# Kernel tuning notes

Measured on AMD Instinct MI355X. Metric: run time of the kernel, lower is better.

Reference implementation:

```python
import jax, jax.numpy as jnp
import numpy as np

INPUT_DIM = 128
DEPTH = 6
HIDDEN = 64
NUM_INNER = 2 ** DEPTH - 1  # 63
NUM_LEAVES = 2 ** DEPTH     # 64


def setup_inputs() -> dict:
    key = jax.random.key(0)
    ks = jax.random.split(key, 6)
    x = jax.random.normal(ks[0], (65536, INPUT_DIM), dtype=jnp.float32)
    s1 = 1.0 / np.sqrt(INPUT_DIM)
    s2 = 1.0 / np.sqrt(HIDDEN)
    W1 = jax.random.uniform(ks[1], (NUM_INNER, INPUT_DIM, HIDDEN), minval=-s1, maxval=s1, dtype=jnp.float32)
    b1 = jax.random.uniform(ks[2], (NUM_INNER, HIDDEN), minval=-s1, maxval=s1, dtype=jnp.float32)
    W2 = jax.random.uniform(ks[3], (NUM_INNER, HIDDEN), minval=-s2, maxval=s2, dtype=jnp.float32)
    b2 = jax.random.uniform(ks[4], (NUM_INNER,), minval=-s2, maxval=s2, dtype=jnp.float32)
    leaf = jax.random.normal(ks[5], (NUM_LEAVES, 1), dtype=jnp.float32)
    return {"x": x, "W1": W1, "b1": b1, "W2": W2, "b2": b2, "leaf": leaf}


def reference(x, W1, b1, W2, b2, leaf):
    # All inner-node MLPs as one batched GEMM pair: [B, N] node probabilities
    h = jax.nn.relu(jnp.einsum('bi,nih->bnh', x, W1) + b1)      # [B, N, H]
    probs = jax.nn.sigmoid(jnp.einsum('bnh,nh->bn', h, W2) + b2)  # [B, N]

    # Original code walks node_idx = 2*node_idx+1 unconditionally, so the chain
    # of used node indices is 2^k - 1 for k = 0..depth-1.
    chain = jnp.array([2 ** k - 1 for k in range(DEPTH)], dtype=jnp.int32)
    p_chain = probs[:, chain]  # [B, D]

    # Bit k (LSB first) of leaf index selects p (bit=1) vs 1-p (bit=0)
    leaves = np.arange(NUM_LEAVES)
    bits = jnp.asarray(((leaves[:, None] >> np.arange(DEPTH)[None, :]) & 1).astype(np.float32))  # [L, D]

    # path_probs[b, l] = prod_k ( bits[l,k]*p + (1-bits[l,k])*(1-p) )
    factors = bits[None, :, :] * p_chain[:, None, :] + (1.0 - bits[None, :, :]) * (1.0 - p_chain[:, None, :])  # [B, L, D]
    path_probs = jnp.prod(factors, axis=-1)  # [B, L]

    return (path_probs @ leaf)[:, 0]  # [B]
```

## Files before the change

kernel.cpp:

```cpp
#include <hip/hip_runtime.h>

typedef __attribute__((ext_vector_type(4))) float f32x4;
typedef __attribute__((ext_vector_type(8))) short bf16x8;
typedef __attribute__((ext_vector_type(4))) unsigned int u32x4;

#define IDIM    128
#define HID     64
#define TDEPTH  6
#define WROWS   32
#define NWAVES  8
#define BLOCK   (NWAVES * 64)
#define MROWS   (WROWS * NWAVES)
#define NODE_ELEMS 8192
#define WFRAG_ELEMS (TDEPTH * NODE_ELEMS)

__device__ __forceinline__ unsigned short f2bf(float f) {
    unsigned int u = __builtin_bit_cast(unsigned int, f);
    unsigned int r = (u + 0x7FFFu + ((u >> 16) & 1u)) >> 16;
    return (unsigned short)r;
}

__device__ __forceinline__ unsigned int f2bf_pk(float f0, float f1) {
    unsigned int u0 = __builtin_bit_cast(unsigned int, f0);
    unsigned int u1 = __builtin_bit_cast(unsigned int, f1);
    unsigned int t0 = u0 + 0x7FFFu + ((u0 >> 16) & 1u);
    unsigned int t1 = u1 + 0x7FFFu + ((u1 >> 16) & 1u);
    return (t1 & 0xFFFF0000u) | (t0 >> 16);
}

__global__ void prep_wfrag(const float* __restrict__ W1, unsigned short* __restrict__ wfrag) {
    int idx = blockIdx.x * 256 + threadIdx.x;
    if (idx >= WFRAG_ELEMS) return;
    int j    = idx & 7;
    int lane = (idx >> 3) & 63;
    int ks   = (idx >> 9) & 3;
    int ht   = (idx >> 11) & 3;
    int nd   = idx >> 13;
    int node = (1 << nd) - 1;
    int k    = ks * 32 + (lane >> 4) * 8 + j;
    int hid  = ht * 16 + (lane & 15);
    wfrag[idx] = f2bf(W1[((size_t)node * IDIM + k) * HID + hid]);
}

template <bool USE_WS>
__global__ __launch_bounds__(BLOCK, 2)
void sdt_kernel(const float* __restrict__ x, const float* __restrict__ W1,
                const float* __restrict__ b1, const float* __restrict__ W2,
                const float* __restrict__ b2, const float* __restrict__ leaf,
                const unsigned short* __restrict__ wfrag, float* __restrict__ out) {
    __shared__ __align__(16) unsigned short bs[TDEPTH * NODE_ELEMS];
    __shared__ float b1s[TDEPTH][HID];
    __shared__ float w2s[TDEPTH][HID];
    __shared__ float b2s[8];
    __shared__ float leaf_lds[64];

    const int tid  = threadIdx.x;
    const int wave = tid >> 6;
    const int lane = tid & 63;
    const int lcol = lane & 15;
    const int lq   = lane >> 4;
    const int m0   = blockIdx.x * MROWS + wave * WROWS;

    const float* xb = x + (size_t)(m0 + lcol) * IDIM + lq * 8;
    float4 araw[2][4][2];
    #pragma unroll
    for (int bg = 0; bg < 2; bg++)
        #pragma unroll
        for (int ks = 0; ks < 4; ks++) {
            const float4* ap = reinterpret_cast<const float4*>(
                xb + (size_t)(bg * 16) * IDIM + ks * 32);
            araw[bg][ks][0] = ap[0];
            araw[bg][ks][1] = ap[1];
        }

    if (USE_WS) {
        const u32x4* src = reinterpret_cast<const u32x4*>(wfrag);
        u32x4* dst = reinterpret_cast<u32x4*>(&bs[0]);
        #pragma unroll
        for (int i = 0; i < (WFRAG_ELEMS * 2 / 16) / BLOCK; i++)
            dst[tid + i * BLOCK] = src[tid + i * BLOCK];
    } else {
        for (int e = tid; e < WFRAG_ELEMS; e += BLOCK) {
            int j = e & 7, ln = (e >> 3) & 63, ks = (e >> 9) & 3,
                ht = (e >> 11) & 3, nd = e >> 13;
            int node = (1 << nd) - 1;
            int k    = ks * 32 + (ln >> 4) * 8 + j;
            int hid  = ht * 16 + (ln & 15);
            bs[e] = f2bf(W1[((size_t)node * IDIM + k) * HID + hid]);
        }
    }
    for (int i = tid; i < TDEPTH * HID; i += BLOCK) {
        int nd = i >> 6, col = i & 63, node = (1 << nd) - 1;
        b1s[nd][col] = b1[node * HID + col];
        w2s[nd][col] = W2[node * HID + col];
    }
    if (tid < 6)  b2s[tid] = b2[(1 << tid) - 1];
    if (tid < 64) leaf_lds[tid] = leaf[tid];

    bf16x8 xfrag[2][4];
    #pragma unroll
    for (int bg = 0; bg < 2; bg++)
        #pragma unroll
        for (int ks = 0; ks < 4; ks++) {
            float4 v0 = araw[bg][ks][0], v1 = araw[bg][ks][1];
            u32x4 pk;
            pk[0] = f2bf_pk(v0.x, v0.y);
            pk[1] = f2bf_pk(v0.z, v0.w);
            pk[2] = f2bf_pk(v1.x, v1.y);
            pk[3] = f2bf_pk(v1.z, v1.w);
            xfrag[bg][ks] = __builtin_bit_cast(bf16x8, pk);
        }

    __syncthreads();

    float pq[2][TDEPTH];

    #pragma unroll
    for (int nd = 0; nd < TDEPTH; nd++) {
        f32x4 acc[2][4];
        #pragma unroll
        for (int bg = 0; bg < 2; bg++)
            #pragma unroll
            for (int ht = 0; ht < 4; ht++)
                acc[bg][ht] = (f32x4){0.f, 0.f, 0.f, 0.f};
        #pragma unroll
        for (int ks = 0; ks < 4; ks++) {
            bf16x8 awf[4];
            #pragma unroll
            for (int ht = 0; ht < 4; ht++)
                awf[ht] = *reinterpret_cast<const bf16x8*>(
                    &bs[(nd * 16 + ht * 4 + ks) * 512 + lane * 8]);
            #pragma unroll
            for (int bg = 0; bg < 2; bg++)
                #pragma unroll
                for (int ht = 0; ht < 4; ht++)
                    acc[bg][ht] = __builtin_amdgcn_mfma_f32_16x16x32_bf16(
                        awf[ht], xfrag[bg][ks], acc[bg][ht], 0, 0, 0);
        }

        f32x4 b1q[4], w2q[4];
        #pragma unroll
        for (int ht = 0; ht < 4; ht++) {
            b1q[ht] = *reinterpret_cast<const f32x4*>(&b1s[nd][ht * 16 + lq * 4]);
            w2q[ht] = *reinterpret_cast<const f32x4*>(&w2s[nd][ht * 16 + lq * 4]);
        }
        const float bias2 = b2s[nd];
        #pragma unroll
        for (int bg = 0; bg < 2; bg++) {
            float s = 0.f;
            #pragma unroll
            for (int ht = 0; ht < 4; ht++)
                #pragma unroll
                for (int r = 0; r < 4; r++) {
                    float v = acc[bg][ht][r] + b1q[ht][r];
                    v = v > 0.f ? v : 0.f;
                    s += v * w2q[ht][r];
                }
            s += __shfl_xor(s, 16, 64);
            s += __shfl_xor(s, 32, 64);
            pq[bg][nd] = 1.f / (1.f + __expf(-(s + bias2)));
        }
    }

    #pragma unroll
    for (int bg = 0; bg < 2; bg++) {
        float q0 = pq[bg][0], q1 = pq[bg][1], q2 = pq[bg][2];
        float q3 = pq[bg][3], p4 = pq[bg][4], p5 = pq[bg][5];
        float acc_out = 0.f;
        #pragma unroll
        for (int ch = 0; ch < 4; ch++) {
            float f4 = (ch & 1) ? p4 : 1.f - p4;
            float f5 = (ch & 2) ? p5 : 1.f - p5;
            const float* lf = leaf_lds + ch * 16;
            float tt[8];
            #pragma unroll
            for (int j = 0; j < 8; j++) {
                float a = lf[2 * j], b = lf[2 * j + 1];
                tt[j] = a + q0 * (b - a);
            }
            #pragma unroll
            for (int j = 0; j < 4; j++) tt[j] = tt[2 * j] + q1 * (tt[2 * j + 1] - tt[2 * j]);
            #pragma unroll
            for (int j = 0; j < 2; j++) tt[j] = tt[2 * j] + q2 * (tt[2 * j + 1] - tt[2 * j]);
            float s = tt[0] + q3 * (tt[1] - tt[0]);
            acc_out += f4 * f5 * s;
        }
        if (lq == 0)
            out[(size_t)m0 + bg * 16 + lcol] = acc_out;
    }
}

extern "C" void kernel_launch(void* const* d_in, const int* in_sizes, int n_in,
                              void* d_out, int out_size, void* d_ws, size_t ws_size,
                              hipStream_t stream) {
    const float* x    = (const float*)d_in[0];
    const float* W1   = (const float*)d_in[1];
    const float* b1   = (const float*)d_in[2];
    const float* W2   = (const float*)d_in[3];
    const float* b2   = (const float*)d_in[4];
    const float* leaf = (const float*)d_in[5];
    float* out = (float*)d_out;

    const int Bn = in_sizes[0] / IDIM;
    const int nblocks = Bn / MROWS;

    if (ws_size >= (size_t)WFRAG_ELEMS * sizeof(unsigned short)) {
        unsigned short* wfrag = (unsigned short*)d_ws;
        prep_wfrag<<<(WFRAG_ELEMS + 255) / 256, 256, 0, stream>>>(W1, wfrag);
        sdt_kernel<true><<<nblocks, BLOCK, 0, stream>>>(x, W1, b1, W2, b2, leaf, wfrag, out);
    } else {
        sdt_kernel<false><<<nblocks, BLOCK, 0, stream>>>(x, W1, b1, W2, b2, leaf, nullptr, out);
    }
}
```

Before: 94.04 us.

## Halve LDS weight buffer with two-phase node staging and smaller blocks

Shrinks the shared-memory weight buffer to hold three tree levels at a time. The second half of the weights is prefetched into registers and written to LDS after the first three nodes are computed. Blocks drop from 8 to 4 waves, and launch bounds now target 3 blocks per CU, to raise occupancy with the smaller LDS footprint. In exchange it adds two extra barriers, register pressure from the prefetched half, and more blocks that each reload the weights.

```diff
diff --git a/kernel.cpp b/kernel.cpp
--- a/kernel.cpp
+++ b/kernel.cpp
@@ -8,11 +8,13 @@
 #define HID     64
 #define TDEPTH  6
 #define WROWS   32
-#define NWAVES  8
+#define NWAVES  4
 #define BLOCK   (NWAVES * 64)
 #define MROWS   (WROWS * NWAVES)
 #define NODE_ELEMS 8192
+#define HALF_ELEMS (3 * NODE_ELEMS)
 #define WFRAG_ELEMS (TDEPTH * NODE_ELEMS)
+#define HALF_VEC (HALF_ELEMS * 2 / 16 / BLOCK)
 
 __device__ __forceinline__ unsigned short f2bf(float f) {
     unsigned int u = __builtin_bit_cast(unsigned int, f);
@@ -43,12 +45,12 @@
 }
 
 template <bool USE_WS>
-__global__ __launch_bounds__(BLOCK, 2)
+__global__ __launch_bounds__(BLOCK, 3)
 void sdt_kernel(const float* __restrict__ x, const float* __restrict__ W1,
                 const float* __restrict__ b1, const float* __restrict__ W2,
                 const float* __restrict__ b2, const float* __restrict__ leaf,
                 const unsigned short* __restrict__ wfrag, float* __restrict__ out) {
-    __shared__ __align__(16) unsigned short bs[TDEPTH * NODE_ELEMS];
+    __shared__ __align__(16) unsigned short bs[HALF_ELEMS];
     __shared__ float b1s[TDEPTH][HID];
     __shared__ float w2s[TDEPTH][HID];
     __shared__ float b2s[8];
@@ -73,14 +75,20 @@
             araw[bg][ks][1] = ap[1];
         }
 
+    u32x4 sB[HALF_VEC];
     if (USE_WS) {
-        const u32x4* src = reinterpret_cast<const u32x4*>(wfrag);
+        const u32x4* srcB = reinterpret_cast<const u32x4*>(wfrag + HALF_ELEMS);
+        #pragma unroll
+        for (int i = 0; i < HALF_VEC; i++) sB[i] = srcB[tid + i * BLOCK];
+    }
+
+    if (USE_WS) {
+        const u32x4* srcA = reinterpret_cast<const u32x4*>(wfrag);
         u32x4* dst = reinterpret_cast<u32x4*>(&bs[0]);
         #pragma unroll
-        for (int i = 0; i < (WFRAG_ELEMS * 2 / 16) / BLOCK; i++)
-            dst[tid + i * BLOCK] = src[tid + i * BLOCK];
+        for (int i = 0; i < HALF_VEC; i++) dst[tid + i * BLOCK] = srcA[tid + i * BLOCK];
     } else {
-        for (int e = tid; e < WFRAG_ELEMS; e += BLOCK) {
+        for (int e = tid; e < HALF_ELEMS; e += BLOCK) {
             int j = e & 7, ln = (e >> 3) & 63, ks = (e >> 9) & 3,
                 ht = (e >> 11) & 3, nd = e >> 13;
             int node = (1 << nd) - 1;
@@ -89,6 +97,7 @@
             bs[e] = f2bf(W1[((size_t)node * IDIM + k) * HID + hid]);
         }
     }
+
     for (int i = tid; i < TDEPTH * HID; i += BLOCK) {
         int nd = i >> 6, col = i & 63, node = (1 << nd) - 1;
         b1s[nd][col] = b1[node * HID + col];
@@ -115,8 +124,7 @@
 
     float pq[2][TDEPTH];
 
-    #pragma unroll
-    for (int nd = 0; nd < TDEPTH; nd++) {
+    auto compute = [&](int nd, int ndl) {
         f32x4 acc[2][4];
         #pragma unroll
         for (int bg = 0; bg < 2; bg++)
@@ -129,7 +137,7 @@
             #pragma unroll
             for (int ht = 0; ht < 4; ht++)
                 awf[ht] = *reinterpret_cast<const bf16x8*>(
-                    &bs[(nd * 16 + ht * 4 + ks) * 512 + lane * 8]);
+                    &bs[(ndl * 16 + ht * 4 + ks) * 512 + lane * 8]);
             #pragma unroll
             for (int bg = 0; bg < 2; bg++)
                 #pragma unroll
@@ -137,7 +145,6 @@
                     acc[bg][ht] = __builtin_amdgcn_mfma_f32_16x16x32_bf16(
                         awf[ht], xfrag[bg][ks], acc[bg][ht], 0, 0, 0);
         }
-
         f32x4 b1q[4], w2q[4];
         #pragma unroll
         for (int ht = 0; ht < 4; ht++) {
@@ -160,7 +167,28 @@
             s += __shfl_xor(s, 32, 64);
             pq[bg][nd] = 1.f / (1.f + __expf(-(s + bias2)));
         }
-    }
+    };
+
+    compute(0, 0); compute(1, 1); compute(2, 2);
+    __syncthreads();
+
+    if (USE_WS) {
+        u32x4* dst = reinterpret_cast<u32x4*>(&bs[0]);
+        #pragma unroll
+        for (int i = 0; i < HALF_VEC; i++) dst[tid + i * BLOCK] = sB[i];
+    } else {
+        for (int e = tid; e < HALF_ELEMS; e += BLOCK) {
+            int j = e & 7, ln = (e >> 3) & 63, ks = (e >> 9) & 3,
+                ht = (e >> 11) & 3, nd = e >> 13;
+            int node = (1 << (nd + 3)) - 1;
+            int k    = ks * 32 + (ln >> 4) * 8 + j;
+            int hid  = ht * 16 + (ln & 15);
+            bs[e] = f2bf(W1[((size_t)node * IDIM + k) * HID + hid]);
+        }
+    }
+    __syncthreads();
+
+    compute(3, 0); compute(4, 1); compute(5, 2);
 
     #pragma unroll
     for (int bg = 0; bg < 2; bg++) {
```

After: 95.28 us. Within noise of the previous version (+1.3%).

## Drop LDS weight staging; single-wave blocks read weight fragments from global/L2

Applied to the files above, without the earlier changes.

Replaces the 8-wave block that staged all six nodes' bf16 weight fragments (96KB) in shared memory with one-wave blocks of 16 rows. Each block reads MFMA weight fragments, biases and leaf values straight from global memory and relies on L1/L2 caching. The goal is to remove the per-block LDS fill and barrier and to lift the occupancy limit set by the large LDS allocation. In exchange, each 16-row wave re-reads the full 96KB of fragments from cache, halves weight reuse per load, and launches 4096 tiny blocks.

```diff
diff --git a/kernel.cpp b/kernel.cpp
--- a/kernel.cpp
+++ b/kernel.cpp
@@ -7,10 +7,8 @@
 #define IDIM    128
 #define HID     64
 #define TDEPTH  6
-#define WROWS   32
-#define NWAVES  8
-#define BLOCK   (NWAVES * 64)
-#define MROWS   (WROWS * NWAVES)
+#define WROWS   16
+#define BLOCK   64
 #define NODE_ELEMS 8192
 #define WFRAG_ELEMS (TDEPTH * NODE_ELEMS)
 
@@ -43,135 +41,103 @@
 }
 
 template <bool USE_WS>
-__global__ __launch_bounds__(BLOCK, 2)
+__global__ __launch_bounds__(BLOCK, 3)
 void sdt_kernel(const float* __restrict__ x, const float* __restrict__ W1,
                 const float* __restrict__ b1, const float* __restrict__ W2,
                 const float* __restrict__ b2, const float* __restrict__ leaf,
                 const unsigned short* __restrict__ wfrag, float* __restrict__ out) {
-    __shared__ __align__(16) unsigned short bs[TDEPTH * NODE_ELEMS];
-    __shared__ float b1s[TDEPTH][HID];
-    __shared__ float w2s[TDEPTH][HID];
-    __shared__ float b2s[8];
-    __shared__ float leaf_lds[64];
-
-    const int tid  = threadIdx.x;
-    const int wave = tid >> 6;
-    const int lane = tid & 63;
+    const int lane = threadIdx.x;
     const int lcol = lane & 15;
     const int lq   = lane >> 4;
-    const int m0   = blockIdx.x * MROWS + wave * WROWS;
+    const int m0   = blockIdx.x * WROWS;
 
     const float* xb = x + (size_t)(m0 + lcol) * IDIM + lq * 8;
-    float4 araw[2][4][2];
+    float4 araw[4][2];
     #pragma unroll
-    for (int bg = 0; bg < 2; bg++)
-        #pragma unroll
-        for (int ks = 0; ks < 4; ks++) {
-            const float4* ap = reinterpret_cast<const float4*>(
-                xb + (size_t)(bg * 16) * IDIM + ks * 32);
-            araw[bg][ks][0] = ap[0];
-            araw[bg][ks][1] = ap[1];
-        }
+    for (int ks = 0; ks < 4; ks++) {
+        const float4* ap = reinterpret_cast<const float4*>(xb + ks * 32);
+        araw[ks][0] = ap[0];
+        araw[ks][1] = ap[1];
+    }
+    bf16x8 xfrag[4];
+    #pragma unroll
+    for (int ks = 0; ks < 4; ks++) {
+        float4 v0 = araw[ks][0], v1 = araw[ks][1];
+        u32x4 pk;
+        pk[0] = f2bf_pk(v0.x, v0.y);
+        pk[1] = f2bf_pk(v0.z, v0.w);
+        pk[2] = f2bf_pk(v1.x, v1.y);
+        pk[3] = f2bf_pk(v1.z, v1.w);
+        xfrag[ks] = __builtin_bit_cast(bf16x8, pk);
+    }
 
-    if (USE_WS) {
-        const u32x4* src = reinterpret_cast<const u32x4*>(wfrag);
-        u32x4* dst = reinterpret_cast<u32x4*>(&bs[0]);
-        #pragma unroll
-        for (int i = 0; i < (WFRAG_ELEMS * 2 / 16) / BLOCK; i++)
-            dst[tid + i * BLOCK] = src[tid + i * BLOCK];
-    } else {
-        for (int e = tid; e < WFRAG_ELEMS; e += BLOCK) {
-            int j = e & 7, ln = (e >> 3) & 63, ks = (e >> 9) & 3,
-                ht = (e >> 11) & 3, nd = e >> 13;
-            int node = (1 << nd) - 1;
-            int k    = ks * 32 + (ln >> 4) * 8 + j;
-            int hid  = ht * 16 + (ln & 15);
-            bs[e] = f2bf(W1[((size_t)node * IDIM + k) * HID + hid]);
-        }
-    }
-    for (int i = tid; i < TDEPTH * HID; i += BLOCK) {
-        int nd = i >> 6, col = i & 63, node = (1 << nd) - 1;
-        b1s[nd][col] = b1[node * HID + col];
-        w2s[nd][col] = W2[node * HID + col];
-    }
-    if (tid < 6)  b2s[tid] = b2[(1 << tid) - 1];
-    if (tid < 64) leaf_lds[tid] = leaf[tid];
-
-    bf16x8 xfrag[2][4];
-    #pragma unroll
-    for (int bg = 0; bg < 2; bg++)
-        #pragma unroll
-        for (int ks = 0; ks < 4; ks++) {
-            float4 v0 = araw[bg][ks][0], v1 = araw[bg][ks][1];
-            u32x4 pk;
-            pk[0] = f2bf_pk(v0.x, v0.y);
-            pk[1] = f2bf_pk(v0.z, v0.w);
-            pk[2] = f2bf_pk(v1.x, v1.y);
-            pk[3] = f2bf_pk(v1.z, v1.w);
-            xfrag[bg][ks] = __builtin_bit_cast(bf16x8, pk);
-        }
-
-    __syncthreads();
-
-    float pq[2][TDEPTH];
+    float pq[TDEPTH];
 
     #pragma unroll
     for (int nd = 0; nd < TDEPTH; nd++) {
-        f32x4 acc[2][4];
+        __builtin_amdgcn_sched_barrier(0);
+        const int node = (1 << nd) - 1;
+
+        f32x4 acc[4];
         #pragma unroll
-        for (int bg = 0; bg < 2; bg++)
-            #pragma unroll
-            for (int ht = 0; ht < 4; ht++)
-                acc[bg][ht] = (f32x4){0.f, 0.f, 0.f, 0.f};
+        for (int ht = 0; ht < 4; ht++)
+            acc[ht] = (f32x4){0.f, 0.f, 0.f, 0.f};
         #pragma unroll
         for (int ks = 0; ks < 4; ks++) {
             bf16x8 awf[4];
+            if (USE_WS) {
+                #pragma unroll
+                for (int ht = 0; ht < 4; ht++)
+                    awf[ht] = *reinterpret_cast<const bf16x8*>(
+                        wfrag + ((nd * 16 + ht * 4 + ks) * 512 + lane * 8));
+            } else {
+                const int k0 = ks * 32 + lq * 8;
+                #pragma unroll
+                for (int ht = 0; ht < 4; ht++) {
+                    const float* wc = W1 + ((size_t)node * IDIM + k0) * HID
+                                    + ht * 16 + lcol;
+                    u32x4 pk;
+                    #pragma unroll
+                    for (int jp = 0; jp < 4; jp++)
+                        pk[jp] = f2bf_pk(wc[(2 * jp) * HID], wc[(2 * jp + 1) * HID]);
+                    awf[ht] = __builtin_bit_cast(bf16x8, pk);
+                }
+            }
             #pragma unroll
             for (int ht = 0; ht < 4; ht++)
-                awf[ht] = *reinterpret_cast<const bf16x8*>(
-                    &bs[(nd * 16 + ht * 4 + ks) * 512 + lane * 8]);
-            #pragma unroll
-            for (int bg = 0; bg < 2; bg++)
-                #pragma unroll
-                for (int ht = 0; ht < 4; ht++)
-                    acc[bg][ht] = __builtin_amdgcn_mfma_f32_16x16x32_bf16(
-                        awf[ht], xfrag[bg][ks], acc[bg][ht], 0, 0, 0);
+                acc[ht] = __builtin_amdgcn_mfma_f32_16x16x32_bf16(
+                    awf[ht], xfrag[ks], acc[ht], 0, 0, 0);
         }
 
-        f32x4 b1q[4], w2q[4];
+        const float bias2 = b2[node];
+        float s = 0.f;
         #pragma unroll
         for (int ht = 0; ht < 4; ht++) {
-            b1q[ht] = *reinterpret_cast<const f32x4*>(&b1s[nd][ht * 16 + lq * 4]);
-            w2q[ht] = *reinterpret_cast<const f32x4*>(&w2s[nd][ht * 16 + lq * 4]);
+            f32x4 b1q = *reinterpret_cast<const f32x4*>(
+                b1 + node * HID + ht * 16 + lq * 4);
+            f32x4 w2q = *reinterpret_cast<const f32x4*>(
+                W2 + node * HID + ht * 16 + lq * 4);
+            #pragma unroll
+            for (int r = 0; r < 4; r++) {
+                float v = acc[ht][r] + b1q[r];
+                v = v > 0.f ? v : 0.f;
+                s += v * w2q[r];
+            }
         }
-        const float bias2 = b2s[nd];
-        #pragma unroll
-        for (int bg = 0; bg < 2; bg++) {
-            float s = 0.f;
-            #pragma unroll
-            for (int ht = 0; ht < 4; ht++)
-                #pragma unroll
-                for (int r = 0; r < 4; r++) {
-                    float v = acc[bg][ht][r] + b1q[ht][r];
-                    v = v > 0.f ? v : 0.f;
-                    s += v * w2q[ht][r];
-                }
-            s += __shfl_xor(s, 16, 64);
-            s += __shfl_xor(s, 32, 64);
-            pq[bg][nd] = 1.f / (1.f + __expf(-(s + bias2)));
-        }
+        s += __shfl_xor(s, 16, 64);
+        s += __shfl_xor(s, 32, 64);
+        pq[nd] = 1.f / (1.f + __expf(-(s + bias2)));
     }
 
-    #pragma unroll
-    for (int bg = 0; bg < 2; bg++) {
-        float q0 = pq[bg][0], q1 = pq[bg][1], q2 = pq[bg][2];
-        float q3 = pq[bg][3], p4 = pq[bg][4], p5 = pq[bg][5];
+    {
+        float q0 = pq[0], q1 = pq[1], q2 = pq[2];
+        float q3 = pq[3], p4 = pq[4], p5 = pq[5];
         float acc_out = 0.f;
         #pragma unroll
         for (int ch = 0; ch < 4; ch++) {
             float f4 = (ch & 1) ? p4 : 1.f - p4;
             float f5 = (ch & 2) ? p5 : 1.f - p5;
-            const float* lf = leaf_lds + ch * 16;
+            const float* lf = leaf + ch * 16;
             float tt[8];
             #pragma unroll
             for (int j = 0; j < 8; j++) {
@@ -182,11 +148,11 @@
             for (int j = 0; j < 4; j++) tt[j] = tt[2 * j] + q1 * (tt[2 * j + 1] - tt[2 * j]);
             #pragma unroll
             for (int j = 0; j < 2; j++) tt[j] = tt[2 * j] + q2 * (tt[2 * j + 1] - tt[2 * j]);
-            float s = tt[0] + q3 * (tt[1] - tt[0]);
-            acc_out += f4 * f5 * s;
+            float sdp = tt[0] + q3 * (tt[1] - tt[0]);
+            acc_out += f4 * f5 * sdp;
         }
         if (lq == 0)
-            out[(size_t)m0 + bg * 16 + lcol] = acc_out;
+            out[(size_t)m0 + lcol] = acc_out;
     }
 }
 
@@ -202,7 +168,7 @@
     float* out = (float*)d_out;
 
     const int Bn = in_sizes[0] / IDIM;
-    const int nblocks = Bn / MROWS;
+    const int nblocks = Bn / WROWS;
 
     if (ws_size >= (size_t)WFRAG_ELEMS * sizeof(unsigned short)) {
         unsigned short* wfrag = (unsigned short*)d_ws;
```

Result: slower. 99.54 us (+5.8%).
